# Kernel optimization log

Measured on AMD Instinct MI355X. Metric: run time of the kernel, lower is better.

## Reference

```python
import jax, jax.numpy as jnp
import numpy as np

N = 8192
DIM = 128


def setup_inputs() -> dict:
    key = jax.random.key(0)
    k1, k2 = jax.random.split(key)
    mapping = jax.random.normal(k1, (N, DIM), dtype=jnp.float32)
    # Cost matrix of the finite metric: symmetric, strictly positive off-diagonal,
    # zero diagonal (the module adds eye to the denominator to handle the diagonal).
    Draw = jax.random.uniform(k2, (N, N), dtype=jnp.float32) * 2.0 + 0.1
    D = 0.5 * (Draw + Draw.T)
    D = D * (1.0 - jnp.eye(N, dtype=jnp.float32))
    return {"mapping": mapping, "D": D}


def reference(mapping, D):
    # Pairwise Euclidean distances via GEMM formulation (||a||^2 - 2ab + ||b||^2)
    # instead of materializing the O(N^2 * dim) broadcast difference.
    n = D.shape[0]
    sq = jnp.sum(mapping * mapping, axis=-1)               # [N]
    gram = mapping @ mapping.T                             # [N, N]
    d2 = sq[:, None] + sq[None, :] - 2.0 * gram            # [N, N]
    d2 = jnp.maximum(d2, 0.0)
    # safe sqrt (exact 0 on the diagonal, matching torch.norm forward)
    pos = d2 > 0
    d = jnp.sqrt(jnp.where(pos, d2, 1.0)) * pos
    ratio = jnp.abs(d - D) / (D + jnp.eye(n, dtype=D.dtype))
    return jnp.sum(ratio) / (n * n - n)
```

## Files before the change

### kernel.cpp

```cpp
#include <hip/hip_runtime.h>
#include <math.h>

#define NN 8192
#define DIM 128
#define NBLK 1024

typedef short bf16x8 __attribute__((ext_vector_type(8)));
typedef float f32x4 __attribute__((ext_vector_type(4)));

__device__ inline void gload_lds16(const void* g, void* l) {
    __builtin_amdgcn_global_load_lds((const __attribute__((address_space(1))) void*)g,
                                     (__attribute__((address_space(3))) void*)l, 16, 0, 0);
}

__device__ inline unsigned short f2bf(float x) {
    unsigned u = __float_as_uint(x);
    unsigned r = u + 0x7FFFu + ((u >> 16) & 1u);
    return (unsigned short)(r >> 16);
}
__device__ inline float bf2f(unsigned short h) {
    return __uint_as_float(((unsigned)h) << 16);
}

__global__ void pack_kernel(const float* __restrict__ m, unsigned short* __restrict__ buf2) {
    const int t = threadIdx.x, l = t & 63;
    const int W = blockIdx.x * 4 + (t >> 6);
    const int g = W >> 2, kq = W & 3;
    const int row = g * 16 + (l & 15);
    const int k0 = kq * 32 + (l >> 4) * 8;
    const float* src = m + (size_t)row * DIM + k0;
    float4 v0 = *reinterpret_cast<const float4*>(src);
    float4 v1 = *reinterpret_cast<const float4*>(src + 4);
    float f[8] = {v0.x, v0.y, v0.z, v0.w, v1.x, v1.y, v1.z, v1.w};
    union { ushort4 u4[2]; unsigned short us[8]; } o;
#pragma unroll
    for (int q = 0; q < 8; ++q) o.us[q] = f2bf(f[q]);
    unsigned short* dst = buf2 + (size_t)W * 512 + l * 8;
    *reinterpret_cast<ushort4*>(dst) = o.u4[0];
    *reinterpret_cast<ushort4*>(dst + 4) = o.u4[1];
}

__global__ void sq_kernel(const float* __restrict__ mapping, float* __restrict__ sq) {
    int i = blockIdx.x * blockDim.x + threadIdx.x;
    if (i < NN) {
        const float4* row = reinterpret_cast<const float4*>(mapping + (size_t)i * DIM);
        float s = 0.f;
#pragma unroll
        for (int q = 0; q < DIM / 4; ++q) {
            float4 v = row[q];
            s += v.x * v.x + v.y * v.y + v.z * v.z + v.w * v.w;
        }
        sq[i] = s;
    }
}

__global__ __launch_bounds__(512, 6) void dist_kernel(const unsigned short* __restrict__ buf2,
                                                      const float* __restrict__ D,
                                                      const float* __restrict__ sq,
                                                      float* __restrict__ partials) {
    __shared__ __align__(16) char Bbuf[2][16384];
    __shared__ __align__(16) char dtile[2][64 * 144];
    __shared__ float wred[8];

    const int t = threadIdx.x, l = t & 63, w = t >> 6;
    const int b = blockIdx.x;
    const int q = b >> 3, p = b & 7;
    const int cj0 = q + p;
    float psum = 0.f;

    if (cj0 < 128) {
        const int nt = ((127 - cj0) >> 3) + 1;
        const int l15 = l & 15, hi = l >> 4;
        const int colq = hi * 4;
        const int strip = w & 3;
        const int i_row = q * 64 + strip * 16 + l15;
        const int ldsoff = (strip * 16 + l15) * 144 + hi * 8;

        if (w < 4) {
            bf16x8 af[4];
#pragma unroll
            for (int kq = 0; kq < 4; ++kq)
                af[kq] = *(const bf16x8*)(buf2 + (size_t)((q * 4 + strip) * 4 + kq) * 512 + l * 8);
            const float sa = sq[i_row];

            f32x4 csb[4], nsb[4];
#pragma unroll
            for (int s = 0; s < 4; ++s)
                csb[s] = *(const f32x4*)(sq + cj0 * 64 + s * 16 + colq);
#pragma unroll
            for (int kq = 0; kq < 4; ++kq)
                gload_lds16(buf2 + (size_t)((cj0 * 4 + strip) * 4 + kq) * 512 + l * 8,
                            (void*)&Bbuf[0][(strip * 4 + kq) * 1024]);
            asm volatile("s_waitcnt vmcnt(0)" ::: "memory");
            __builtin_amdgcn_s_barrier();

            for (int tt = 0; tt < nt; ++tt) {
                const int slot = tt & 1;
                if (tt + 1 < nt) {
                    const int ncj = cj0 + (tt + 1) * 8;
#pragma unroll
                    for (int s = 0; s < 4; ++s)
                        nsb[s] = *(const f32x4*)(sq + ncj * 64 + s * 16 + colq);
#pragma unroll
                    for (int kq = 0; kq < 4; ++kq)
                        gload_lds16(buf2 + (size_t)((ncj * 4 + strip) * 4 + kq) * 512 + l * 8,
                                    (void*)&Bbuf[slot ^ 1][(strip * 4 + kq) * 1024]);
                }
#pragma unroll
                for (int s = 0; s < 4; ++s) {
                    bf16x8 bfr[4];
#pragma unroll
                    for (int kq = 0; kq < 4; ++kq)
                        bfr[kq] = *(const bf16x8*)&Bbuf[slot][(s * 4 + kq) * 1024 + l * 16];
                    f32x4 acc = {};
#pragma unroll
                    for (int kq = 0; kq < 4; ++kq)
                        acc = __builtin_amdgcn_mfma_f32_16x16x32_bf16(bfr[kq], af[kq], acc, 0, 0, 0);
                    ushort4 o;
                    unsigned short* op = (unsigned short*)&o;
#pragma unroll
                    for (int r = 0; r < 4; ++r) {
                        float d2 = fmaf(-2.f, acc[r], sa + csb[s][r]);
                        op[r] = f2bf(sqrtf(fmaxf(d2, 0.f)));
                    }
                    *reinterpret_cast<ushort4*>(&dtile[slot][0] + ldsoff + s * 32) = o;
                }
                asm volatile("s_waitcnt vmcnt(0) lgkmcnt(0)" ::: "memory");
                __builtin_amdgcn_sched_barrier(0);
                __builtin_amdgcn_s_barrier();
                if (tt + 1 < nt) {
#pragma unroll
                    for (int s = 0; s < 4; ++s) csb[s] = nsb[s];
                }
            }
        } else {
            const float* Drow = D + (size_t)i_row * NN;

            auto consume = [&](int tile, const f32x4(&dc)[4]) {
                const int cj = cj0 + tile * 8;
                const char* slot = &dtile[tile & 1][0];
                if (cj != q) {
#pragma unroll
                    for (int s = 0; s < 4; ++s) {
                        ushort4 o = *reinterpret_cast<const ushort4*>(slot + ldsoff + s * 32);
                        const unsigned short* op = (const unsigned short*)&o;
#pragma unroll
                        for (int r = 0; r < 4; ++r) {
                            float Dv = dc[s][r];
                            psum += __fdividef(fabsf(bf2f(op[r]) - Dv), Dv);
                        }
                    }
                } else {
#pragma unroll
                    for (int s = 0; s < 4; ++s) {
                        ushort4 o = *reinterpret_cast<const ushort4*>(slot + ldsoff + s * 32);
                        const unsigned short* op = (const unsigned short*)&o;
#pragma unroll
                        for (int r = 0; r < 4; ++r) {
                            const int j = cj * 64 + s * 16 + colq + r;
                            if (j > i_row) {
                                float Dv = dc[s][r];
                                psum += __fdividef(fabsf(bf2f(op[r]) - Dv), Dv);
                            }
                        }
                    }
                }
            };

            f32x4 dA[4], dB[4];
#pragma unroll
            for (int s = 0; s < 4; ++s)
                dA[s] = *(const f32x4*)(Drow + cj0 * 64 + s * 16 + colq);
            __builtin_amdgcn_s_barrier();

            bool cur_a = true;
            for (int tt = 0; tt < nt; ++tt) {
                if (tt + 1 < nt) {
                    const int ncj = cj0 + (tt + 1) * 8;
                    if (cur_a) {
#pragma unroll
                        for (int s = 0; s < 4; ++s)
                            dB[s] = *(const f32x4*)(Drow + ncj * 64 + s * 16 + colq);
                    } else {
#pragma unroll
                        for (int s = 0; s < 4; ++s)
                            dA[s] = *(const f32x4*)(Drow + ncj * 64 + s * 16 + colq);
                    }
                }
                __builtin_amdgcn_s_barrier();
                if (cur_a) consume(tt, dA);
                else       consume(tt, dB);
                cur_a = !cur_a;
            }
        }
    }

    for (int off = 32; off > 0; off >>= 1) psum += __shfl_down(psum, off, 64);
    __syncthreads();
    if (l == 0) wred[w] = psum;
    __syncthreads();
    if (t == 0) {
        float s = 0.f;
#pragma unroll
        for (int k = 0; k < 8; ++k) s += wred[k];
        partials[b] = 2.f * s;
    }
}

__global__ void reduce_kernel(const float* __restrict__ partials, float* __restrict__ out) {
    __shared__ double sm[256];
    const int t = threadIdx.x;
    double s = 0.0;
    for (int i = t; i < NBLK; i += 256) s += (double)partials[i];
    sm[t] = s;
    __syncthreads();
    for (int off = 128; off > 0; off >>= 1) {
        if (t < off) sm[t] += sm[t + off];
        __syncthreads();
    }
    if (t == 0) out[0] = (float)(sm[0] / ((double)NN * (double)NN - (double)NN));
}

extern "C" void kernel_launch(void* const* d_in, const int* in_sizes, int n_in,
                              void* d_out, int out_size, void* d_ws, size_t ws_size,
                              hipStream_t stream) {
    const float* mapping = (const float*)d_in[0];
    const float* D       = (const float*)d_in[1];
    float* out = (float*)d_out;

    unsigned short* buf2 = (unsigned short*)d_ws;
    float* sq            = (float*)(buf2 + NN * DIM);
    float* partials      = sq + NN;

    pack_kernel<<<512, 256, 0, stream>>>(mapping, buf2);
    sq_kernel<<<NN / 256, 256, 0, stream>>>(mapping, sq);
    dist_kernel<<<NBLK, 512, 0, stream>>>(buf2, D, sq, partials);
    reduce_kernel<<<1, 256, 0, stream>>>(partials, out);
}
```

Baseline: 65.94 us.

## Fuse squared-norm into pack, last-block final reduce, move sqrt to consumer

Squared row norms are now computed inside the pack kernel using shuffles and shared memory, which removes the separate sq_kernel launch. The final reduction moves into dist_kernel: a global atomic counter picks the last block, and that block sums the partials, so reduce_kernel goes away. A memset is added to reset the counter. The sqrt moves from the MFMA producer waves to the D-consumer waves, and d2 rather than d is stored in bf16, which changes rounding and may shift accuracy.

New measurement: 85.92 us. 1.3x slower.

```diff
diff --git a/kernel.cpp b/kernel.cpp
--- a/kernel.cpp
+++ b/kernel.cpp
@@ -22,10 +22,12 @@
     return __uint_as_float(((unsigned)h) << 16);
 }
 
-__global__ void pack_kernel(const float* __restrict__ m, unsigned short* __restrict__ buf2) {
+__global__ void pack_kernel(const float* __restrict__ m, unsigned short* __restrict__ buf2,
+                            float* __restrict__ sq) {
     const int t = threadIdx.x, l = t & 63;
-    const int W = blockIdx.x * 4 + (t >> 6);
-    const int g = W >> 2, kq = W & 3;
+    const int kq = t >> 6;
+    const int g = blockIdx.x;
+    const int W = g * 4 + kq;
     const int row = g * 16 + (l & 15);
     const int k0 = kq * 32 + (l >> 4) * 8;
     const float* src = m + (size_t)row * DIM + k0;
@@ -33,34 +35,34 @@
     float4 v1 = *reinterpret_cast<const float4*>(src + 4);
     float f[8] = {v0.x, v0.y, v0.z, v0.w, v1.x, v1.y, v1.z, v1.w};
     union { ushort4 u4[2]; unsigned short us[8]; } o;
-#pragma unroll
-    for (int q = 0; q < 8; ++q) o.us[q] = f2bf(f[q]);
+    float s = 0.f;
+#pragma unroll
+    for (int q = 0; q < 8; ++q) {
+        o.us[q] = f2bf(f[q]);
+        s += f[q] * f[q];
+    }
     unsigned short* dst = buf2 + (size_t)W * 512 + l * 8;
     *reinterpret_cast<ushort4*>(dst) = o.u4[0];
     *reinterpret_cast<ushort4*>(dst + 4) = o.u4[1];
-}
-
-__global__ void sq_kernel(const float* __restrict__ mapping, float* __restrict__ sq) {
-    int i = blockIdx.x * blockDim.x + threadIdx.x;
-    if (i < NN) {
-        const float4* row = reinterpret_cast<const float4*>(mapping + (size_t)i * DIM);
-        float s = 0.f;
-#pragma unroll
-        for (int q = 0; q < DIM / 4; ++q) {
-            float4 v = row[q];
-            s += v.x * v.x + v.y * v.y + v.z * v.z + v.w * v.w;
-        }
-        sq[i] = s;
-    }
+
+    s += __shfl_xor(s, 16, 64);
+    s += __shfl_xor(s, 32, 64);
+    __shared__ float sqp[4][16];
+    if ((l >> 4) == 0) sqp[kq][l & 15] = s;
+    __syncthreads();
+    if (t < 16) sq[g * 16 + t] = (sqp[0][t] + sqp[1][t]) + (sqp[2][t] + sqp[3][t]);
 }
 
 __global__ __launch_bounds__(512, 6) void dist_kernel(const unsigned short* __restrict__ buf2,
                                                       const float* __restrict__ D,
                                                       const float* __restrict__ sq,
-                                                      float* __restrict__ partials) {
+                                                      float* __restrict__ partials,
+                                                      unsigned int* __restrict__ counter,
+                                                      float* __restrict__ out) {
     __shared__ __align__(16) char Bbuf[2][16384];
     __shared__ __align__(16) char dtile[2][64 * 144];
     __shared__ float wred[8];
+    __shared__ int islast;
 
     const int t = threadIdx.x, l = t & 63, w = t >> 6;
     const int b = blockIdx.x;
@@ -121,7 +123,7 @@
 #pragma unroll
                     for (int r = 0; r < 4; ++r) {
                         float d2 = fmaf(-2.f, acc[r], sa + csb[s][r]);
-                        op[r] = f2bf(sqrtf(fmaxf(d2, 0.f)));
+                        op[r] = f2bf(fmaxf(d2, 0.f));
                     }
                     *reinterpret_cast<ushort4*>(&dtile[slot][0] + ldsoff + s * 32) = o;
                 }
@@ -146,8 +148,9 @@
                         const unsigned short* op = (const unsigned short*)&o;
 #pragma unroll
                         for (int r = 0; r < 4; ++r) {
+                            float d = sqrtf(bf2f(op[r]));
                             float Dv = dc[s][r];
-                            psum += __fdividef(fabsf(bf2f(op[r]) - Dv), Dv);
+                            psum += __fdividef(fabsf(d - Dv), Dv);
                         }
                     }
                 } else {
@@ -159,8 +162,9 @@
                         for (int r = 0; r < 4; ++r) {
                             const int j = cj * 64 + s * 16 + colq + r;
                             if (j > i_row) {
+                                float d = sqrtf(bf2f(op[r]));
                                 float Dv = dc[s][r];
-                                psum += __fdividef(fabsf(bf2f(op[r]) - Dv), Dv);
+                                psum += __fdividef(fabsf(d - Dv), Dv);
                             }
                         }
                     }
@@ -204,21 +208,25 @@
 #pragma unroll
         for (int k = 0; k < 8; ++k) s += wred[k];
         partials[b] = 2.f * s;
-    }
-}
-
-__global__ void reduce_kernel(const float* __restrict__ partials, float* __restrict__ out) {
-    __shared__ double sm[256];
-    const int t = threadIdx.x;
-    double s = 0.0;
-    for (int i = t; i < NBLK; i += 256) s += (double)partials[i];
-    sm[t] = s;
-    __syncthreads();
-    for (int off = 128; off > 0; off >>= 1) {
-        if (t < off) sm[t] += sm[t + off];
+        __threadfence();
+        unsigned int old = atomicAdd(counter, 1u);
+        islast = (old == NBLK - 1);
+    }
+    __syncthreads();
+
+    if (islast) {
+        __threadfence();
+        double* red = (double*)&Bbuf[0][0];
+        double s = 0.0;
+        for (int i = t; i < NBLK; i += 512) s += (double)partials[i];
+        red[t] = s;
         __syncthreads();
-    }
-    if (t == 0) out[0] = (float)(sm[0] / ((double)NN * (double)NN - (double)NN));
+        for (int off = 256; off > 0; off >>= 1) {
+            if (t < off) red[t] += red[t + off];
+            __syncthreads();
+        }
+        if (t == 0) out[0] = (float)(red[0] / ((double)NN * (double)NN - (double)NN));
+    }
 }
 
 extern "C" void kernel_launch(void* const* d_in, const int* in_sizes, int n_in,
@@ -231,9 +239,9 @@
     unsigned short* buf2 = (unsigned short*)d_ws;
     float* sq            = (float*)(buf2 + NN * DIM);
     float* partials      = sq + NN;
-
-    pack_kernel<<<512, 256, 0, stream>>>(mapping, buf2);
-    sq_kernel<<<NN / 256, 256, 0, stream>>>(mapping, sq);
-    dist_kernel<<<NBLK, 512, 0, stream>>>(buf2, D, sq, partials);
-    reduce_kernel<<<1, 256, 0, stream>>>(partials, out);
-}
+    unsigned int* counter = (unsigned int*)(partials + NBLK);
+
+    hipMemsetAsync(counter, 0, sizeof(unsigned int), stream);
+    pack_kernel<<<512, 256, 0, stream>>>(mapping, buf2, sq);
+    dist_kernel<<<NBLK, 512, 0, stream>>>(buf2, D, sq, partials, counter, out);
+}
```
